# Performance work log

Measured on AMD Instinct MI355X. Metric: run time of the kernel, lower is better.

The kernel has to match this reference:

```python
import math
import jax, jax.numpy as jnp
import numpy as np

NUM_HEADS = 32
NUM_KV_HEADS = 8
HEAD_SIZE = 128
FEATURE_DIM = 64
SEQ_LEN = 2048
WINDOW_SIZE = 64
EPS = 1e-12
MASK_VALUE = -100000000.0


def _make_masks(n: int, w: int):
    # block-diagonal ones(w,w) tiles, plus the rolled (sub-diagonal) tiles
    m = math.ceil(n / w)
    mask = np.kron(np.eye(m), np.ones((w, w)))
    mask = mask + np.roll(mask, -w, axis=-1)
    mask = mask[:n, :n]
    mask_window = np.tril(mask).astype(bool)[None, None]          # [1,1,n,n]
    mask_linear = np.tril(1.0 - mask).astype(bool)[None, None]    # [1,1,n,n]
    return jnp.asarray(mask_window), jnp.asarray(mask_linear)


def _feature_map(w, x):
    # f(x) = clamp(cat(softmax(xW), softmax(-xW)), min=eps)
    z = jnp.einsum('hdf,bhld->bhlf', w, x)
    return jnp.clip(
        jnp.concatenate([jax.nn.softmax(z, axis=-1), jax.nn.softmax(-z, axis=-1)], axis=-1),
        EPS, None)


def setup_inputs() -> dict:
    key = jax.random.key(0)
    ks = jax.random.split(key, 6)
    return {
        'query': jax.random.normal(ks[0], (SEQ_LEN, NUM_HEADS * HEAD_SIZE), dtype=jnp.float32),
        'key': jax.random.normal(ks[1], (SEQ_LEN, NUM_KV_HEADS * HEAD_SIZE), dtype=jnp.float32),
        'value': jax.random.normal(ks[2], (SEQ_LEN, NUM_KV_HEADS * HEAD_SIZE), dtype=jnp.float32),
        'fmap_q_w': 0.02 * jax.random.normal(ks[3], (NUM_HEADS, HEAD_SIZE, FEATURE_DIM), dtype=jnp.float32),
        'fmap_k_w': 0.02 * jax.random.normal(ks[4], (NUM_HEADS, HEAD_SIZE, FEATURE_DIM), dtype=jnp.float32),
        'window_factors': jax.random.normal(ks[5], (1, NUM_HEADS, 1, 1), dtype=jnp.float32),
    }


def reference(query, key, value, fmap_q_w, fmap_k_w, window_factors):
    T = query.shape[0]
    q = query.reshape(T, NUM_HEADS, HEAD_SIZE)
    k = key.reshape(T, NUM_KV_HEADS, HEAD_SIZE)
    v = value.reshape(T, NUM_KV_HEADS, HEAD_SIZE)
    rep = NUM_HEADS // NUM_KV_HEADS
    k = jnp.repeat(k, rep, axis=1)
    v = jnp.repeat(v, rep, axis=1)
    # [T,H,D] -> [1,H,T,D]
    q = jnp.moveaxis(q, 0, -2)[None]
    k = jnp.moveaxis(k, 0, -2)[None]
    v = jnp.moveaxis(v, 0, -2)[None]

    f_q = _feature_map(fmap_q_w, q)  # [1,H,T,2F]
    f_k = _feature_map(fmap_k_w, k)
    wf = jax.nn.sigmoid(window_factors)

    mask_window, mask_linear = _make_masks(SEQ_LEN, WINDOW_SIZE)
    mask_window = mask_window[:, :, :T, :T]
    mask_linear = mask_linear[:, :, :T, :T]

    # sliding-window softmax term
    a_sm = jnp.einsum('bhmd,bhnd->bhmn', q, k) * (HEAD_SIZE ** -0.5)
    a_sm = jnp.where(mask_window, a_sm, MASK_VALUE)
    a_sm_max = jnp.max(a_sm, axis=-1, keepdims=True)
    a_sm = wf * jnp.exp(a_sm - a_sm_max)
    sum_sm = jnp.sum(a_sm, axis=-1, keepdims=True)

    # linear feature-map term (linear_factor = 1)
    a_ln = jnp.einsum('bhmd,bhnd->bhmn', f_q, f_k)
    a_ln = jnp.where(mask_linear, a_ln, 0.0)
    sum_ln = jnp.sum(a_ln, axis=-1, keepdims=True)

    y = jnp.einsum('bhmn,bhnd->bhmd', a_sm + a_ln, v)
    return y / (sum_sm + sum_ln)
```

## Files before the change

### kernel.cpp

```cpp
#include <hip/hip_runtime.h>
#include <math.h>

#define T_SEQ 2048
#define NH    32
#define NKV   8
#define HS    128
#define FD    64
#define NBLK  32
#define EPSF  1e-12f
#define LDP   136

typedef unsigned short u16;
typedef __bf16 bf16x8 __attribute__((ext_vector_type(8)));
typedef float  f32x4  __attribute__((ext_vector_type(4)));

__device__ __forceinline__ u16 f2b(float f) {
  unsigned u = __builtin_bit_cast(unsigned, f);
  return (u16)((u + 0x7fffu + ((u >> 16) & 1u)) >> 16);
}

#define FQB_OFF 0
#define FKT_OFF 16777216
#define ST_OFF  33554432
#define VT_OFF  71303168
#define WT_OFF  75497472

__global__ __launch_bounds__(256) void k_wt(
    const float* __restrict__ wq, const float* __restrict__ wk, u16* __restrict__ WT)
{
  __shared__ float sW[128 * 68];
  const int h = blockIdx.x, isk = blockIdx.y, tid = threadIdx.x;
  const float* src = (isk ? wk : wq) + (size_t)h * HS * FD;
  for (int idx = tid * 4; idx < 8192; idx += 1024) {
    int r = idx >> 6, c = idx & 63;
    *(float4*)(sW + r * 68 + c) = *(const float4*)(src + idx);
  }
  __syncthreads();
  u16* dst = WT + ((size_t)(isk * NH + h)) * 8192;
  for (int i = 0; i < 8; ++i) {
    int ch = tid + i * 256;
    int f = ch >> 5, d4 = (ch & 31) * 4;
    ushort4 u;
    u.x = f2b(sW[(d4 + 0) * 68 + f]);
    u.y = f2b(sW[(d4 + 1) * 68 + f]);
    u.z = f2b(sW[(d4 + 2) * 68 + f]);
    u.w = f2b(sW[(d4 + 3) * 68 + f]);
    *(ushort4*)(dst + f * 128 + d4) = u;
  }
}

__global__ __launch_bounds__(256) void k_fmap(
    const float* __restrict__ qg, const float* __restrict__ kg,
    const u16* __restrict__ WT,
    u16* __restrict__ fqb, u16* __restrict__ FKT)
{
  __shared__ __align__(16) u16 smem[2 * 64 * 136];
  u16* sX = smem;
  u16* sW = smem + 64 * 136;
  const int lt = blockIdx.x, h = blockIdx.y, isk = blockIdx.z;
  const int tid = threadIdx.x, lane = tid & 63, w = tid >> 6;
  const int quad = lane >> 4, txn = lane & 15;

  const float* xbase = isk ? (kg + (h >> 2) * HS) : (qg + h * HS);
  const int    xstr  = isk ? (NKV * HS) : (NH * HS);
  for (int idx = tid * 4; idx < 8192; idx += 1024) {
    int r = idx >> 7, c = idx & 127;
    float4 v4 = *(const float4*)(xbase + (size_t)(lt * 64 + r) * xstr + c);
    ushort4 u; u.x = f2b(v4.x); u.y = f2b(v4.y); u.z = f2b(v4.z); u.w = f2b(v4.w);
    *(ushort4*)(sX + r * 136 + c) = u;
  }
  const u16* wt = WT + ((size_t)(isk * NH + h)) * 8192;
  for (int i = 0; i < 4; ++i) {
    int ch = tid + i * 256;
    int row = ch >> 4, d8 = (ch & 15) * 8;
    *(uint4*)(sW + row * 136 + d8) = *(const uint4*)(wt + row * 128 + d8);
  }
  __syncthreads();

  const int arow = w * 16 + txn;
  const f32x4 vzero = {0.f, 0.f, 0.f, 0.f};
  f32x4 zt[4] = {vzero, vzero, vzero, vzero};
#pragma unroll
  for (int ks = 0; ks < 4; ++ks) {
    bf16x8 a = *(const bf16x8*)(sX + arow * 136 + ks * 32 + quad * 8);
#pragma unroll
    for (int nt = 0; nt < 4; ++nt) {
      bf16x8 bb = *(const bf16x8*)(sW + (nt * 16 + txn) * 136 + ks * 32 + quad * 8);
      zt[nt] = __builtin_amdgcn_mfma_f32_16x16x32_bf16(a, bb, zt[nt], 0, 0, 0);
    }
  }

  float E1[4][4], E2[4][4];
#pragma unroll
  for (int r = 0; r < 4; ++r) {
    float zv[4];
    float mx = -1e30f, mn = 1e30f;
#pragma unroll
    for (int nt = 0; nt < 4; ++nt) {
      zv[nt] = zt[nt][r];
      mx = fmaxf(mx, zv[nt]); mn = fminf(mn, zv[nt]);
    }
#pragma unroll
    for (int o = 1; o < 16; o <<= 1) {
      mx = fmaxf(mx, __shfl_xor(mx, o));
      mn = fminf(mn, __shfl_xor(mn, o));
    }
    float e1[4], e2[4], s1 = 0.f, s2 = 0.f;
#pragma unroll
    for (int nt = 0; nt < 4; ++nt) {
      e1[nt] = __expf(zv[nt] - mx); s1 += e1[nt];
      e2[nt] = __expf(mn - zv[nt]); s2 += e2[nt];
    }
#pragma unroll
    for (int o = 1; o < 16; o <<= 1) { s1 += __shfl_xor(s1, o); s2 += __shfl_xor(s2, o); }
    float r1 = 1.f / s1, r2 = 1.f / s2;
#pragma unroll
    for (int nt = 0; nt < 4; ++nt) {
      E1[r][nt] = fmaxf(e1[nt] * r1, EPSF);
      E2[r][nt] = fmaxf(e2[nt] * r2, EPSF);
    }
  }

  __syncthreads();

  if (!isk) {
#pragma unroll
    for (int r = 0; r < 4; ++r) {
      int row = w * 16 + quad * 4 + r;
#pragma unroll
      for (int nt = 0; nt < 4; ++nt) {
        sX[row * 136 + nt * 16 + txn]      = f2b(E1[r][nt]);
        sX[row * 136 + 64 + nt * 16 + txn] = f2b(E2[r][nt]);
      }
    }
    __syncthreads();
    u16* ob = fqb + ((size_t)(h * NBLK + lt)) * 8192;
    for (int i = 0; i < 4; ++i) {
      int ch = tid + i * 256;
      int row = ch >> 4, f8 = (ch & 15) * 8;
      *(uint4*)(ob + row * 128 + f8) = *(const uint4*)(sX + row * 136 + f8);
    }
  } else {
#pragma unroll
    for (int r = 0; r < 4; ++r) {
      int j = w * 16 + quad * 4 + r;
#pragma unroll
      for (int nt = 0; nt < 4; ++nt) {
        sX[(nt * 16 + txn) * 68 + j]        = f2b(E1[r][nt]);
        sX[(nt * 16 + txn + 64) * 68 + j]   = f2b(E2[r][nt]);
      }
    }
    __syncthreads();
    u16* ob = FKT + (size_t)h * 128 * T_SEQ + lt * 64;
    for (int i = 0; i < 8; ++i) {
      int ch = tid + i * 256;
      int row = ch >> 4, j4 = (ch & 15) * 4;
      *(ushort4*)(ob + (size_t)row * T_SEQ + j4) = *(const ushort4*)(sX + row * 68 + j4);
    }
  }
}

__global__ __launch_bounds__(256) void k_vt(const float* __restrict__ vg, u16* __restrict__ VT)
{
  __shared__ float sV[64 * 129];
  const int b = blockIdx.x, kvh = blockIdx.y, tid = threadIdx.x;
  for (int idx = tid * 4; idx < 8192; idx += 1024) {
    int r = idx >> 7, c = idx & 127;
    *(float4*)(sV + r * 129 + c) = *(const float4*)(vg + (size_t)(b * 64 + r) * (NKV * HS) + kvh * HS + c);
  }
  __syncthreads();
  const int lane = tid & 63, w = tid >> 6;
#pragma unroll
  for (int i = 0; i < 32; ++i) {
    int d = w * 32 + i;
    VT[((size_t)(kvh * 128 + d)) * T_SEQ + b * 64 + lane] = f2b(sV[lane * 129 + d]);
  }
}

__global__ __launch_bounds__(256) void k_scan(
    const u16* __restrict__ FKT, const u16* __restrict__ VT, u16* __restrict__ ST)
{
  __shared__ __align__(16) u16 sVT[16 * 72];
  __shared__ __align__(16) u16 sFK[64 * 72];
  __shared__ __align__(16) u16 sOne[16 * 72];
  __shared__ __align__(16) u16 sO[16 * 72];
  const int dc = blockIdx.x, fh = blockIdx.y, h = blockIdx.z;
  const int tid = threadIdx.x, lane = tid & 63, w = tid >> 6;
  const int quad = lane >> 4, txn = lane & 15;
  const bool doz = (dc == 0);

  for (int idx = tid * 8; idx < 16 * 72; idx += 2048) {
    ushort4 o4; o4.x = 0x3F80; o4.y = 0x3F80; o4.z = 0x3F80; o4.w = 0x3F80;
    *(ushort4*)(sOne + idx) = o4;
    *(ushort4*)(sOne + idx + 4) = o4;
  }

  const u16* vbase = VT + ((size_t)((h >> 2) * 128 + dc * 16)) * T_SEQ;
  const u16* fbase = FKT + ((size_t)(h * 128 + fh * 64)) * T_SEQ;

  const int srow = tid >> 4, sj4 = (tid & 15) * 4;
  ushort4 rv, rf[4];
  rv = *(const ushort4*)(vbase + (size_t)srow * T_SEQ + sj4);
#pragma unroll
  for (int i = 0; i < 4; ++i) {
    int ch = tid + i * 256;
    int fr = ch >> 4, fj4 = (ch & 15) * 4;
    rf[i] = *(const ushort4*)(fbase + (size_t)fr * T_SEQ + fj4);
  }

  const f32x4 vzero = {0.f, 0.f, 0.f, 0.f};
  f32x4 acc = vzero, zacc = vzero;

  for (int b = 0; b < NBLK; ++b) {
    __syncthreads();
    *(ushort4*)(sVT + srow * 72 + sj4) = rv;
#pragma unroll
    for (int i = 0; i < 4; ++i) {
      int ch = tid + i * 256;
      int fr = ch >> 4, fj4 = (ch & 15) * 4;
      *(ushort4*)(sFK + fr * 72 + fj4) = rf[i];
    }
    __syncthreads();
    if (b + 1 < NBLK) {
      rv = *(const ushort4*)(vbase + (size_t)srow * T_SEQ + (b + 1) * 64 + sj4);
#pragma unroll
      for (int i = 0; i < 4; ++i) {
        int ch = tid + i * 256;
        int fr = ch >> 4, fj4 = (ch & 15) * 4;
        rf[i] = *(const ushort4*)(fbase + (size_t)fr * T_SEQ + (b + 1) * 64 + fj4);
      }
    }
#pragma unroll
    for (int ks = 0; ks < 2; ++ks) {
      bf16x8 a  = *(const bf16x8*)(sVT + txn * 72 + ks * 32 + quad * 8);
      bf16x8 bb = *(const bf16x8*)(sFK + (w * 16 + txn) * 72 + ks * 32 + quad * 8);
      acc = __builtin_amdgcn_mfma_f32_16x16x32_bf16(a, bb, acc, 0, 0, 0);
      if (doz) {
        bf16x8 ao = *(const bf16x8*)(sOne + txn * 72 + ks * 32 + quad * 8);
        zacc = __builtin_amdgcn_mfma_f32_16x16x32_bf16(ao, bb, zacc, 0, 0, 0);
      }
    }
#pragma unroll
    for (int r = 0; r < 4; ++r)
      sO[(quad * 4 + r) * 72 + w * 16 + txn] = f2b(acc[r]);
    if (doz && quad == 0)
      ST[(((size_t)(h * NBLK + b)) * 144 + 128) * 128 + fh * 64 + w * 16 + txn] = f2b(zacc[0]);
    __syncthreads();
    *(ushort4*)(ST + (((size_t)(h * NBLK + b)) * 144 + dc * 16 + srow) * 128 + fh * 64 + sj4)
        = *(const ushort4*)(sO + srow * 72 + sj4);
  }
}

__global__ __launch_bounds__(256, 3) void k_main(
    const float* __restrict__ qg, const float* __restrict__ kg,
    const u16* __restrict__ fqb, const u16* __restrict__ ST, const u16* __restrict__ VT,
    const float* __restrict__ wfac, float* __restrict__ out)
{
  __shared__ u16 RA[64 * LDP];
  __shared__ u16 RB[128 * LDP];
  const int B = blockIdx.x, h = blockIdx.y, tid = threadIdx.x;
  const int lane = tid & 63, w = tid >> 6;
  const int quad = lane >> 4, txn = lane & 15;
  const int arow = w * 16 + txn;
  const int koff = quad * 8;

  const f32x4 vzero = {0.f, 0.f, 0.f, 0.f};
  f32x4 y[8];
#pragma unroll
  for (int t = 0; t < 8; ++t) y[t] = vzero;
  float sln[4] = {0.f, 0.f, 0.f, 0.f};

  if (B >= 2) {
    const u16* fsrc = fqb + ((size_t)(h * NBLK + B)) * 8192;
    for (int idx = tid * 4; idx < 8192; idx += 1024) {
      int r = idx >> 7, c = idx & 127;
      *(ushort4*)(RA + r * LDP + c) = *(const ushort4*)(fsrc + idx);
    }
    const u16* ssrc = ST + ((size_t)(h * NBLK + (B - 2))) * 18432;
    for (int idx = tid * 4; idx < 8192; idx += 1024) {
      int r = idx >> 7, c = idx & 127;
      *(ushort4*)(RB + r * LDP + c) = *(const ushort4*)(ssrc + idx);
    }
    __syncthreads();
    f32x4 a8 = vzero;
#pragma unroll
    for (int ks = 0; ks < 4; ++ks) {
      bf16x8 a = *(const bf16x8*)(RA + arow * LDP + ks * 32 + koff);
#pragma unroll
      for (int t = 0; t < 4; ++t) {
        bf16x8 bb = *(const bf16x8*)(RB + (t * 16 + txn) * LDP + ks * 32 + koff);
        y[t] = __builtin_amdgcn_mfma_f32_16x16x32_bf16(a, bb, y[t], 0, 0, 0);
      }
    }
    __syncthreads();
    for (int idx = tid * 4; idx < 10240; idx += 1024) {
      int r = idx >> 7, c = idx & 127;
      *(ushort4*)(RB + r * LDP + c) = *(const ushort4*)(ssrc + 8192 + idx);
    }
    __syncthreads();
#pragma unroll
    for (int ks = 0; ks < 4; ++ks) {
      bf16x8 a = *(const bf16x8*)(RA + arow * LDP + ks * 32 + koff);
#pragma unroll
      for (int t = 4; t < 8; ++t) {
        bf16x8 bb = *(const bf16x8*)(RB + (t * 16 + txn - 64) * LDP + ks * 32 + koff);
        y[t] = __builtin_amdgcn_mfma_f32_16x16x32_bf16(a, bb, y[t], 0, 0, 0);
      }
      bf16x8 b8 = *(const bf16x8*)(RB + (64 + txn) * LDP + ks * 32 + koff);
      a8 = __builtin_amdgcn_mfma_f32_16x16x32_bf16(a, b8, a8, 0, 0, 0);
    }
#pragma unroll
    for (int r = 0; r < 4; ++r) sln[r] = __shfl(a8[r], lane & 48);
    __syncthreads();
  }

  const int kb0 = (B >= 1) ? B - 1 : 0;
  {
    const float* qs = qg + (size_t)(B * 64) * (NH * HS) + h * HS;
    for (int idx = tid * 4; idx < 8192; idx += 1024) {
      int r = idx >> 7, c = idx & 127;
      float4 v4 = *(const float4*)(qs + (size_t)r * (NH * HS) + c);
      ushort4 u; u.x = f2b(v4.x); u.y = f2b(v4.y); u.z = f2b(v4.z); u.w = f2b(v4.w);
      *(ushort4*)(RA + r * LDP + c) = u;
    }
    for (int idx = tid * 4; idx < 16384; idx += 1024) {
      int r = idx >> 7, c = idx & 127;
      int key = (r < 64) ? (kb0 * 64 + r) : (B * 64 + (r - 64));
      float4 v4 = *(const float4*)(kg + (size_t)key * (NKV * HS) + (h >> 2) * HS + c);
      ushort4 u; u.x = f2b(v4.x); u.y = f2b(v4.y); u.z = f2b(v4.z); u.w = f2b(v4.w);
      *(ushort4*)(RB + r * LDP + c) = u;
    }
  }
  __syncthreads();

  f32x4 s[8];
#pragma unroll
  for (int t = 0; t < 8; ++t) s[t] = vzero;
#pragma unroll
  for (int ks = 0; ks < 4; ++ks) {
    bf16x8 a = *(const bf16x8*)(RA + arow * LDP + ks * 32 + koff);
#pragma unroll
    for (int t = 0; t < 8; ++t) {
      bf16x8 bb = *(const bf16x8*)(RB + (t * 16 + txn) * LDP + ks * 32 + koff);
      s[t] = __builtin_amdgcn_mfma_f32_16x16x32_bf16(a, bb, s[t], 0, 0, 0);
    }
  }

  float wf = wfac[h];
  wf = 1.f / (1.f + __expf(-wf));
  const float scale = 0.08838834764831845f;
  float ssum[4];
#pragma unroll
  for (int r = 0; r < 4; ++r) {
    const int irow = w * 16 + quad * 4 + r;
    float sv[8];
    float m = -1e30f;
#pragma unroll
    for (int t = 0; t < 8; ++t) {
      float x = s[t][r] * scale;
      bool msk = (t < 4) ? (B == 0) : ((t - 4) * 16 + txn > irow);
      x = msk ? -1e30f : x;
      sv[t] = x;
      m = fmaxf(m, x);
    }
#pragma unroll
    for (int o = 1; o < 16; o <<= 1) m = fmaxf(m, __shfl_xor(m, o));
    float ss = 0.f;
#pragma unroll
    for (int t = 0; t < 8; ++t) {
      float e = (sv[t] > -1e29f) ? wf * __expf(sv[t] - m) : 0.f;
      ss += e;
      RA[irow * LDP + t * 16 + txn] = f2b(e);
    }
#pragma unroll
    for (int o = 1; o < 16; o <<= 1) ss += __shfl_xor(ss, o);
    ssum[r] = ss;
  }
  __syncthreads();

  {
    const u16* vts = VT + (size_t)((h >> 2) * 128) * T_SEQ;
    for (int idx = tid * 4; idx < 16384; idx += 1024) {
      int r = idx >> 7, c = idx & 127;
      int key = (c < 64) ? (kb0 * 64 + c) : (B * 64 + (c - 64));
      *(ushort4*)(RB + r * LDP + c) = *(const ushort4*)(vts + (size_t)r * T_SEQ + key);
    }
  }
  __syncthreads();

#pragma unroll
  for (int ks = 0; ks < 4; ++ks) {
    if (B == 0 && ks < 2) continue;
    bf16x8 a = *(const bf16x8*)(RA + arow * LDP + ks * 32 + koff);
#pragma unroll
    for (int t = 0; t < 8; ++t) {
      bf16x8 bb = *(const bf16x8*)(RB + (t * 16 + txn) * LDP + ks * 32 + koff);
      y[t] = __builtin_amdgcn_mfma_f32_16x16x32_bf16(a, bb, y[t], 0, 0, 0);
    }
  }

  const size_t obase = ((size_t)h * T_SEQ + B * 64) * HS;
#pragma unroll
  for (int r = 0; r < 4; ++r) {
    float inv = 1.f / (ssum[r] + sln[r]);
    int irow = w * 16 + quad * 4 + r;
#pragma unroll
    for (int t = 0; t < 8; ++t)
      out[obase + (size_t)irow * HS + t * 16 + txn] = y[t][r] * inv;
  }
}

extern "C" void kernel_launch(void* const* d_in, const int* in_sizes, int n_in,
                              void* d_out, int out_size, void* d_ws, size_t ws_size,
                              hipStream_t stream) {
  const float* q    = (const float*)d_in[0];
  const float* k    = (const float*)d_in[1];
  const float* v    = (const float*)d_in[2];
  const float* wq   = (const float*)d_in[3];
  const float* wk   = (const float*)d_in[4];
  const float* wfac = (const float*)d_in[5];
  float* out = (float*)d_out;
  char* wsb = (char*)d_ws;

  u16* fqb = (u16*)(wsb + FQB_OFF);
  u16* FKT = (u16*)(wsb + FKT_OFF);
  u16* ST  = (u16*)(wsb + ST_OFF);
  u16* VT  = (u16*)(wsb + VT_OFF);
  u16* WT  = (u16*)(wsb + WT_OFF);

  k_wt   <<<dim3(NH, 2),       256, 0, stream>>>(wq, wk, WT);
  k_vt   <<<dim3(NBLK, NKV),   256, 0, stream>>>(v, VT);
  k_fmap <<<dim3(NBLK, NH, 2), 256, 0, stream>>>(q, k, WT, fqb, FKT);
  k_scan <<<dim3(8, 2, NH),    256, 0, stream>>>(FKT, VT, ST);
  k_main <<<dim3(NBLK, NH),    256, 0, stream>>>(q, k, fqb, ST, VT, wfac, out);
}
```

Measured before the change: 197.8 us.

## Fuse weight and value prep kernels, halve k_main LDS for higher occupancy

Merges the weight-transpose and value-transpose kernels into a single launch, saving one kernel launch. In the main kernel, the RB shared buffer is halved: the two key blocks and the two V^T halves are now staged one after the other with extra barriers, and the normalizer row comes from a small side buffer through a masked MFMA. Launch bounds go from 3 to 4 blocks per CU so more workgroups can be resident. The cost is extra synchronizations and serialized load/compute phases inside each block.

```diff
diff --git a/kernel.cpp b/kernel.cpp
--- a/kernel.cpp
+++ b/kernel.cpp
@@ -25,27 +25,48 @@
 #define VT_OFF  71303168
 #define WT_OFF  75497472
 
-__global__ __launch_bounds__(256) void k_wt(
-    const float* __restrict__ wq, const float* __restrict__ wk, u16* __restrict__ WT)
+__global__ __launch_bounds__(256) void k_pre(
+    const float* __restrict__ wq, const float* __restrict__ wk,
+    const float* __restrict__ vg,
+    u16* __restrict__ WT, u16* __restrict__ VT)
 {
-  __shared__ float sW[128 * 68];
-  const int h = blockIdx.x, isk = blockIdx.y, tid = threadIdx.x;
-  const float* src = (isk ? wk : wq) + (size_t)h * HS * FD;
-  for (int idx = tid * 4; idx < 8192; idx += 1024) {
-    int r = idx >> 6, c = idx & 63;
-    *(float4*)(sW + r * 68 + c) = *(const float4*)(src + idx);
-  }
-  __syncthreads();
-  u16* dst = WT + ((size_t)(isk * NH + h)) * 8192;
-  for (int i = 0; i < 8; ++i) {
-    int ch = tid + i * 256;
-    int f = ch >> 5, d4 = (ch & 31) * 4;
-    ushort4 u;
-    u.x = f2b(sW[(d4 + 0) * 68 + f]);
-    u.y = f2b(sW[(d4 + 1) * 68 + f]);
-    u.z = f2b(sW[(d4 + 2) * 68 + f]);
-    u.w = f2b(sW[(d4 + 3) * 68 + f]);
-    *(ushort4*)(dst + f * 128 + d4) = u;
+  __shared__ float sB[128 * 68];
+  const int bx = blockIdx.x, tid = threadIdx.x;
+
+  if (bx < 64) {
+    const int h = bx >> 1, isk = bx & 1;
+    const float* src = (isk ? wk : wq) + (size_t)h * HS * FD;
+    for (int idx = tid * 4; idx < 8192; idx += 1024) {
+      int r = idx >> 6, c = idx & 63;
+      *(float4*)(sB + r * 68 + c) = *(const float4*)(src + idx);
+    }
+    __syncthreads();
+    u16* dst = WT + ((size_t)(isk * NH + h)) * 8192;
+    for (int i = 0; i < 8; ++i) {
+      int ch = tid + i * 256;
+      int f = ch >> 5, d4 = (ch & 31) * 4;
+      ushort4 u;
+      u.x = f2b(sB[(d4 + 0) * 68 + f]);
+      u.y = f2b(sB[(d4 + 1) * 68 + f]);
+      u.z = f2b(sB[(d4 + 2) * 68 + f]);
+      u.w = f2b(sB[(d4 + 3) * 68 + f]);
+      *(ushort4*)(dst + f * 128 + d4) = u;
+    }
+  } else {
+    const int idx2 = bx - 64;
+    const int b = idx2 & 31, kvh = idx2 >> 5;
+    float* sV = sB;
+    for (int idx = tid * 4; idx < 8192; idx += 1024) {
+      int r = idx >> 7, c = idx & 127;
+      *(float4*)(sV + r * 129 + c) = *(const float4*)(vg + (size_t)(b * 64 + r) * (NKV * HS) + kvh * HS + c);
+    }
+    __syncthreads();
+    const int lane = tid & 63, w = tid >> 6;
+#pragma unroll
+    for (int i = 0; i < 32; ++i) {
+      int d = w * 32 + i;
+      VT[((size_t)(kvh * 128 + d)) * T_SEQ + b * 64 + lane] = f2b(sV[lane * 129 + d]);
+    }
   }
 }
 
@@ -160,23 +181,6 @@
   }
 }
 
-__global__ __launch_bounds__(256) void k_vt(const float* __restrict__ vg, u16* __restrict__ VT)
-{
-  __shared__ float sV[64 * 129];
-  const int b = blockIdx.x, kvh = blockIdx.y, tid = threadIdx.x;
-  for (int idx = tid * 4; idx < 8192; idx += 1024) {
-    int r = idx >> 7, c = idx & 127;
-    *(float4*)(sV + r * 129 + c) = *(const float4*)(vg + (size_t)(b * 64 + r) * (NKV * HS) + kvh * HS + c);
-  }
-  __syncthreads();
-  const int lane = tid & 63, w = tid >> 6;
-#pragma unroll
-  for (int i = 0; i < 32; ++i) {
-    int d = w * 32 + i;
-    VT[((size_t)(kvh * 128 + d)) * T_SEQ + b * 64 + lane] = f2b(sV[lane * 129 + d]);
-  }
-}
-
 __global__ __launch_bounds__(256) void k_scan(
     const u16* __restrict__ FKT, const u16* __restrict__ VT, u16* __restrict__ ST)
 {
@@ -251,13 +255,14 @@
   }
 }
 
-__global__ __launch_bounds__(256, 3) void k_main(
+__global__ __launch_bounds__(256, 4) void k_main(
     const float* __restrict__ qg, const float* __restrict__ kg,
     const u16* __restrict__ fqb, const u16* __restrict__ ST, const u16* __restrict__ VT,
     const float* __restrict__ wfac, float* __restrict__ out)
 {
-  __shared__ u16 RA[64 * LDP];
-  __shared__ u16 RB[128 * LDP];
+  __shared__ __align__(16) u16 RA[64 * LDP];
+  __shared__ __align__(16) u16 RB[64 * LDP];
+  __shared__ __align__(16) u16 sz[128];
   const int B = blockIdx.x, h = blockIdx.y, tid = threadIdx.x;
   const int lane = tid & 63, w = tid >> 6;
   const int quad = lane >> 4, txn = lane & 15;
@@ -269,6 +274,7 @@
 #pragma unroll
   for (int t = 0; t < 8; ++t) y[t] = vzero;
   float sln[4] = {0.f, 0.f, 0.f, 0.f};
+  const bf16x8 bzero = {0, 0, 0, 0, 0, 0, 0, 0};
 
   if (B >= 2) {
     const u16* fsrc = fqb + ((size_t)(h * NBLK + B)) * 8192;
@@ -281,8 +287,9 @@
       int r = idx >> 7, c = idx & 127;
       *(ushort4*)(RB + r * LDP + c) = *(const ushort4*)(ssrc + idx);
     }
-    __syncthreads();
-    f32x4 a8 = vzero;
+    if (tid < 32) *(ushort4*)(sz + tid * 4) = *(const ushort4*)(ssrc + 16384 + tid * 4);
+    __syncthreads();
+    f32x4 yz = vzero;
 #pragma unroll
     for (int ks = 0; ks < 4; ++ks) {
       bf16x8 a = *(const bf16x8*)(RA + arow * LDP + ks * 32 + koff);
@@ -291,9 +298,11 @@
         bf16x8 bb = *(const bf16x8*)(RB + (t * 16 + txn) * LDP + ks * 32 + koff);
         y[t] = __builtin_amdgcn_mfma_f32_16x16x32_bf16(a, bb, y[t], 0, 0, 0);
       }
-    }
-    __syncthreads();
-    for (int idx = tid * 4; idx < 10240; idx += 1024) {
+      bf16x8 bz = (txn == 0) ? *(const bf16x8*)(sz + ks * 32 + koff) : bzero;
+      yz = __builtin_amdgcn_mfma_f32_16x16x32_bf16(a, bz, yz, 0, 0, 0);
+    }
+    __syncthreads();
+    for (int idx = tid * 4; idx < 8192; idx += 1024) {
       int r = idx >> 7, c = idx & 127;
       *(ushort4*)(RB + r * LDP + c) = *(const ushort4*)(ssrc + 8192 + idx);
     }
@@ -306,11 +315,9 @@
         bf16x8 bb = *(const bf16x8*)(RB + (t * 16 + txn - 64) * LDP + ks * 32 + koff);
         y[t] = __builtin_amdgcn_mfma_f32_16x16x32_bf16(a, bb, y[t], 0, 0, 0);
       }
-      bf16x8 b8 = *(const bf16x8*)(RB + (64 + txn) * LDP + ks * 32 + koff);
-      a8 = __builtin_amdgcn_mfma_f32_16x16x32_bf16(a, b8, a8, 0, 0, 0);
-    }
-#pragma unroll
-    for (int r = 0; r < 4; ++r) sln[r] = __shfl(a8[r], lane & 48);
+    }
+#pragma unroll
+    for (int r = 0; r < 4; ++r) sln[r] = __shfl(yz[r], lane & 48);
     __syncthreads();
   }
 
@@ -323,10 +330,10 @@
       ushort4 u; u.x = f2b(v4.x); u.y = f2b(v4.y); u.z = f2b(v4.z); u.w = f2b(v4.w);
       *(ushort4*)(RA + r * LDP + c) = u;
     }
-    for (int idx = tid * 4; idx < 16384; idx += 1024) {
-      int r = idx >> 7, c = idx & 127;
-      int key = (r < 64) ? (kb0 * 64 + r) : (B * 64 + (r - 64));
-      float4 v4 = *(const float4*)(kg + (size_t)key * (NKV * HS) + (h >> 2) * HS + c);
+    const float* kd = kg + (size_t)(B * 64) * (NKV * HS) + (h >> 2) * HS;
+    for (int idx = tid * 4; idx < 8192; idx += 1024) {
+      int r = idx >> 7, c = idx & 127;
+      float4 v4 = *(const float4*)(kd + (size_t)r * (NKV * HS) + c);
       ushort4 u; u.x = f2b(v4.x); u.y = f2b(v4.y); u.z = f2b(v4.z); u.w = f2b(v4.w);
       *(ushort4*)(RB + r * LDP + c) = u;
     }
@@ -340,9 +347,30 @@
   for (int ks = 0; ks < 4; ++ks) {
     bf16x8 a = *(const bf16x8*)(RA + arow * LDP + ks * 32 + koff);
 #pragma unroll
-    for (int t = 0; t < 8; ++t) {
+    for (int t = 0; t < 4; ++t) {
       bf16x8 bb = *(const bf16x8*)(RB + (t * 16 + txn) * LDP + ks * 32 + koff);
-      s[t] = __builtin_amdgcn_mfma_f32_16x16x32_bf16(a, bb, s[t], 0, 0, 0);
+      s[4 + t] = __builtin_amdgcn_mfma_f32_16x16x32_bf16(a, bb, s[4 + t], 0, 0, 0);
+    }
+  }
+
+  if (B >= 1) {
+    __syncthreads();
+    const float* kd = kg + (size_t)(kb0 * 64) * (NKV * HS) + (h >> 2) * HS;
+    for (int idx = tid * 4; idx < 8192; idx += 1024) {
+      int r = idx >> 7, c = idx & 127;
+      float4 v4 = *(const float4*)(kd + (size_t)r * (NKV * HS) + c);
+      ushort4 u; u.x = f2b(v4.x); u.y = f2b(v4.y); u.z = f2b(v4.z); u.w = f2b(v4.w);
+      *(ushort4*)(RB + r * LDP + c) = u;
+    }
+    __syncthreads();
+#pragma unroll
+    for (int ks = 0; ks < 4; ++ks) {
+      bf16x8 a = *(const bf16x8*)(RA + arow * LDP + ks * 32 + koff);
+#pragma unroll
+      for (int t = 0; t < 4; ++t) {
+        bf16x8 bb = *(const bf16x8*)(RB + (t * 16 + txn) * LDP + ks * 32 + koff);
+        s[t] = __builtin_amdgcn_mfma_f32_16x16x32_bf16(a, bb, s[t], 0, 0, 0);
+      }
     }
   }
 
@@ -378,23 +406,38 @@
   }
   __syncthreads();
 
-  {
-    const u16* vts = VT + (size_t)((h >> 2) * 128) * T_SEQ;
-    for (int idx = tid * 4; idx < 16384; idx += 1024) {
-      int r = idx >> 7, c = idx & 127;
-      int key = (c < 64) ? (kb0 * 64 + c) : (B * 64 + (c - 64));
-      *(ushort4*)(RB + r * LDP + c) = *(const ushort4*)(vts + (size_t)r * T_SEQ + key);
-    }
-  }
-  __syncthreads();
-
+  const u16* vts = VT + (size_t)((h >> 2) * 128) * T_SEQ;
+  for (int idx = tid * 4; idx < 8192; idx += 1024) {
+    int r = idx >> 7, c = idx & 127;
+    int key = (c < 64) ? (kb0 * 64 + c) : (B * 64 + (c - 64));
+    *(ushort4*)(RB + r * LDP + c) = *(const ushort4*)(vts + (size_t)r * T_SEQ + key);
+  }
+  __syncthreads();
 #pragma unroll
   for (int ks = 0; ks < 4; ++ks) {
     if (B == 0 && ks < 2) continue;
     bf16x8 a = *(const bf16x8*)(RA + arow * LDP + ks * 32 + koff);
 #pragma unroll
-    for (int t = 0; t < 8; ++t) {
+    for (int t = 0; t < 4; ++t) {
       bf16x8 bb = *(const bf16x8*)(RB + (t * 16 + txn) * LDP + ks * 32 + koff);
+      y[t] = __builtin_amdgcn_mfma_f32_16x16x32_bf16(a, bb, y[t], 0, 0, 0);
+    }
+  }
+  __syncthreads();
+
+  for (int idx = tid * 4; idx < 8192; idx += 1024) {
+    int r = idx >> 7, c = idx & 127;
+    int key = (c < 64) ? (kb0 * 64 + c) : (B * 64 + (c - 64));
+    *(ushort4*)(RB + r * LDP + c) = *(const ushort4*)(vts + (size_t)(r + 64) * T_SEQ + key);
+  }
+  __syncthreads();
+#pragma unroll
+  for (int ks = 0; ks < 4; ++ks) {
+    if (B == 0 && ks < 2) continue;
+    bf16x8 a = *(const bf16x8*)(RA + arow * LDP + ks * 32 + koff);
+#pragma unroll
+    for (int t = 4; t < 8; ++t) {
+      bf16x8 bb = *(const bf16x8*)(RB + (t * 16 + txn - 64) * LDP + ks * 32 + koff);
       y[t] = __builtin_amdgcn_mfma_f32_16x16x32_bf16(a, bb, y[t], 0, 0, 0);
     }
   }
@@ -428,8 +471,7 @@
   u16* VT  = (u16*)(wsb + VT_OFF);
   u16* WT  = (u16*)(wsb + WT_OFF);
 
-  k_wt   <<<dim3(NH, 2),       256, 0, stream>>>(wq, wk, WT);
-  k_vt   <<<dim3(NBLK, NKV),   256, 0, stream>>>(v, VT);
+  k_pre  <<<dim3(320),         256, 0, stream>>>(wq, wk, v, WT, VT);
   k_fmap <<<dim3(NBLK, NH, 2), 256, 0, stream>>>(q, k, WT, fqb, FKT);
   k_scan <<<dim3(8, 2, NH),    256, 0, stream>>>(FKT, VT, ST);
   k_main <<<dim3(NBLK, NH),    256, 0, stream>>>(q, k, fqb, ST, VT, wfac, out);
```

New measurement: 176.9 us. 10.6% less time.
